# Performance work log

Measured on AMD Instinct MI355X. Metric: run time of the kernel, lower is better.

## Reference

```python
import jax, jax.numpy as jnp
import numpy as np

PRUNE_N = 2  # entries zeroed per group
PRUNE_M = 4  # group size along feature dim


def _prune_2of4(x_flat):
    # x_flat: [N, D]; zero out the PRUNE_N smallest-|.| entries in every
    # contiguous group of PRUNE_M columns (matches torch topk(largest=False)
    # + scatter mask semantics, deterministic sort-order tie-breaking).
    N, D = x_flat.shape
    g = x_flat.reshape(N, D // PRUNE_M, PRUNE_M)           # [N, G, 4]
    a = jnp.abs(g)
    order = jnp.argsort(a, axis=-1)                         # ascending |.|
    rank = jnp.argsort(order, axis=-1)                      # rank of each slot
    keep = rank >= PRUNE_N                                  # keep 2 largest
    return jnp.where(keep, g, jnp.zeros_like(g)).reshape(N, D)


def setup_inputs() -> dict:
    key = jax.random.key(0)
    k1, k2 = jax.random.split(key)
    B, S, D_IN, D_OUT = 2, 4096, 4096, 4096
    x = jax.random.normal(k1, (B, S, D_IN), dtype=jnp.float32)
    weight = jax.random.normal(k2, (D_OUT, D_IN), dtype=jnp.float32) * 0.02
    return {"x": x, "weight": weight}


def reference(x, weight):
    B, S, D = x.shape
    x_flat = x.reshape(B * S, D)
    x_sp = _prune_2of4(x_flat)                              # [B*S, D]
    out = x_sp @ weight.T                                   # [B*S, D_out]
    return out
```

## Files before the change

### kernel.cpp

```cpp
#include <hip/hip_runtime.h>
#include <hip/hip_bf16.h>

typedef float f32x4 __attribute__((ext_vector_type(4)));
typedef __bf16 bf16x8 __attribute__((ext_vector_type(8)));
typedef unsigned short ushort_t;
typedef ushort_t u16x8 __attribute__((ext_vector_type(8)));

__device__ inline ushort_t f2bf_rne(float f) {
  unsigned u = __builtin_bit_cast(unsigned, f);
  unsigned r = (u + 0x7fffu + ((u >> 16) & 1u)) >> 16;
  return (ushort_t)r;
}

__global__ void prune_cast_kernel(const float* __restrict__ x,
                                  ushort_t* __restrict__ xsp, long n8) {
  long i = (long)blockIdx.x * blockDim.x + threadIdx.x;
  if (i >= n8) return;
  const float4* p = reinterpret_cast<const float4*>(x);
  float4 g0 = p[2 * i];
  float4 g1 = p[2 * i + 1];
  float v[8] = {g0.x, g0.y, g0.z, g0.w, g1.x, g1.y, g1.z, g1.w};
  u16x8 o;
#pragma unroll
  for (int g = 0; g < 2; ++g) {
    float a[4];
#pragma unroll
    for (int j = 0; j < 4; ++j) a[j] = fabsf(v[g * 4 + j]);
#pragma unroll
    for (int j = 0; j < 4; ++j) {
      int rank = 0;
#pragma unroll
      for (int k = 0; k < 4; ++k) {
        if (k == j) continue;
        rank += (a[k] < a[j]) || (a[k] == a[j] && k < j);
      }
      o[g * 4 + j] = (rank >= 2) ? f2bf_rne(v[g * 4 + j]) : (ushort_t)0;
    }
  }
  reinterpret_cast<u16x8*>(xsp)[i] = o;
}

__global__ void cast_bf16_kernel(const float* __restrict__ w,
                                 ushort_t* __restrict__ wb, long n8) {
  long i = (long)blockIdx.x * blockDim.x + threadIdx.x;
  if (i >= n8) return;
  const float4* p = reinterpret_cast<const float4*>(w);
  float4 g0 = p[2 * i];
  float4 g1 = p[2 * i + 1];
  u16x8 o;
  o[0] = f2bf_rne(g0.x); o[1] = f2bf_rne(g0.y);
  o[2] = f2bf_rne(g0.z); o[3] = f2bf_rne(g0.w);
  o[4] = f2bf_rne(g1.x); o[5] = f2bf_rne(g1.y);
  o[6] = f2bf_rne(g1.z); o[7] = f2bf_rne(g1.w);
  reinterpret_cast<u16x8*>(wb)[i] = o;
}

#define BARM()                              \
  asm volatile("" ::: "memory");            \
  __builtin_amdgcn_s_barrier();             \
  asm volatile("" ::: "memory");
#define WAIT_VM0() asm volatile("s_waitcnt vmcnt(0)" ::: "memory")

#define STAGE_A(t1, h, par)                                                    \
  {                                                                            \
    const ushort_t* g0 =                                                       \
        A + (a_row0 + (h) * 128 + srow) * (long)Kd + (t1) * 64 + scol;         \
    const ushort_t* g1 =                                                       \
        A + (a_row0 + (h) * 128 + srow + 8) * (long)Kd + (t1) * 64 + scol;     \
    ushort_t* l0 = &ldsA[((par) * 2 + (h)) * 8192 + w * 1024];                 \
    __builtin_amdgcn_global_load_lds(                                          \
        (const __attribute__((address_space(1))) void*)g0,                     \
        (__attribute__((address_space(3))) void*)l0, 16, 0, 0);                \
    __builtin_amdgcn_global_load_lds(                                          \
        (const __attribute__((address_space(1))) void*)g1,                     \
        (__attribute__((address_space(3))) void*)(l0 + 512), 16, 0, 0);        \
  }

#define STAGE_B(t1, h, par)                                                    \
  {                                                                            \
    const ushort_t* g0 =                                                       \
        B + (b_row0 + (h) * 128 + srow) * (long)Kd + (t1) * 64 + scol;         \
    const ushort_t* g1 =                                                       \
        B + (b_row0 + (h) * 128 + srow + 8) * (long)Kd + (t1) * 64 + scol;     \
    ushort_t* l0 = &ldsB[((par) * 2 + (h)) * 8192 + w * 1024];                 \
    __builtin_amdgcn_global_load_lds(                                          \
        (const __attribute__((address_space(1))) void*)g0,                     \
        (__attribute__((address_space(3))) void*)l0, 16, 0, 0);                \
    __builtin_amdgcn_global_load_lds(                                          \
        (const __attribute__((address_space(1))) void*)g1,                     \
        (__attribute__((address_space(3))) void*)(l0 + 512), 16, 0, 0);        \
  }

#define LDA_FRAG(dst, par, mi, s)                                              \
  dst = *reinterpret_cast<const bf16x8*>(                                      \
      reinterpret_cast<const char*>(ldsA) + ((par) * 2 + wr) * 16384 +         \
      (mi) * 2048 + ((s) ? roff1 : roff0));

#define LDB_FRAG(dst, par, ni, s)                                              \
  dst = *reinterpret_cast<const bf16x8*>(                                      \
      reinterpret_cast<const char*>(ldsB) + ((par) * 2 + (wc >> 1)) * 16384 +  \
      (wc & 1) * 8192 + (ni) * 2048 + ((s) ? roff1 : roff0));

#define MFMA_Q(MH, NH)                                                         \
  __builtin_amdgcn_s_setprio(1);                                               \
  _Pragma("unroll") for (int s = 0; s < 2; ++s)                                \
  _Pragma("unroll") for (int mi = 0; mi < 4; ++mi)                             \
  _Pragma("unroll") for (int ni = 0; ni < 2; ++ni)                             \
      acc[(MH) * 4 + mi][(NH) * 2 + ni] =                                      \
          __builtin_amdgcn_mfma_f32_16x16x32_bf16(                             \
              af[mi][s], bfr[(NH) * 2 + ni][s],                                \
              acc[(MH) * 4 + mi][(NH) * 2 + ni], 0, 0, 0);                     \
  __builtin_amdgcn_s_setprio(0);

#define KTILE(t, PAR)                                                          \
  {                                                                            \
    const int tN = ((t) + 1 < NT) ? (t) + 1 : NT - 1;                          \
           \
    STAGE_A(tN, 0, (PAR) ^ 1)                                                  \
    STAGE_A(tN, 1, (PAR) ^ 1)                                                  \
    STAGE_B(tN, 0, (PAR) ^ 1)                                                  \
    STAGE_B(tN, 1, (PAR) ^ 1)                                                  \
                          \
    _Pragma("unroll") for (int mi = 0; mi < 4; ++mi)                           \
    _Pragma("unroll") for (int s = 0; s < 2; ++s)                              \
        LDA_FRAG(af[mi][s], PAR, mi, s)                                        \
    _Pragma("unroll") for (int ni = 0; ni < 4; ++ni)                           \
    _Pragma("unroll") for (int s = 0; s < 2; ++s)                              \
        LDB_FRAG(bfr[ni][s], PAR, ni, s)                                       \
    MFMA_Q(0, 0)                                                               \
    MFMA_Q(0, 1)                                                               \
    _Pragma("unroll") for (int mi = 0; mi < 4; ++mi)                           \
    _Pragma("unroll") for (int s = 0; s < 2; ++s)                              \
        LDA_FRAG(af[mi][s], PAR, 4 + mi, s)                                    \
    MFMA_Q(1, 1)                                                               \
    MFMA_Q(1, 0)                                                               \
    WAIT_VM0();                                                                \
    BARM()                                                                     \
  }

__global__ __launch_bounds__(512, 1) void gemm256_kernel(
    const ushort_t* __restrict__ A,
    const ushort_t* __restrict__ B,
    float* __restrict__ C,
    int M, int N, int Kd) {
  __shared__ ushort_t ldsA[4 * 8192];
  __shared__ ushort_t ldsB[4 * 8192];

  const int tid = threadIdx.x;
  const int lane = tid & 63;
  const int w = tid >> 6;
  const int wr = w >> 2;
  const int wc = w & 3;

  const int b = blockIdx.x;
  const int wg = (b & 7) * (gridDim.x >> 3) + (b >> 3);
  const int nbn = N / 256;
  const int bm = wg / nbn, bn = wg % nbn;
  const long a_row0 = (long)bm * 256;
  const long b_row0 = (long)bn * 256;
  const int NT = Kd / 64;

  const int srow = w * 16 + (lane >> 3);
  const int scol = (((lane & 7) ^ ((lane >> 3) & 7)) << 3);

  const int rl = lane & 15;
  const int q = lane >> 4;
  const int roff0 = rl * 128 + (((q) ^ (rl & 7)) << 4);
  const int roff1 = rl * 128 + (((q | 4) ^ (rl & 7)) << 4);

  f32x4 acc[8][4];
#pragma unroll
  for (int i = 0; i < 8; ++i)
#pragma unroll
    for (int j = 0; j < 4; ++j) acc[i][j] = f32x4{0.f, 0.f, 0.f, 0.f};

  bf16x8 af[4][2];
  bf16x8 bfr[4][2];

  STAGE_A(0, 0, 0)
  STAGE_A(0, 1, 0)
  STAGE_B(0, 0, 0)
  STAGE_B(0, 1, 0)
  WAIT_VM0();
  BARM()

  for (int t = 0; t < NT; t += 2) {
    KTILE(t, 0)
    KTILE(t + 1, 1)
  }

  const int orow = (lane >> 4) * 4;
  const int ocol = lane & 15;
#pragma unroll
  for (int mi = 0; mi < 8; ++mi)
#pragma unroll
    for (int ni = 0; ni < 4; ++ni) {
      const long r0 = a_row0 + wr * 128 + mi * 16 + orow;
      const long c0 = b_row0 + wc * 64 + ni * 16 + ocol;
#pragma unroll
      for (int r = 0; r < 4; ++r) C[(r0 + r) * N + c0] = acc[mi][ni][r];
    }
}

extern "C" void kernel_launch(void* const* d_in, const int* in_sizes, int n_in,
                              void* d_out, int out_size, void* d_ws,
                              size_t ws_size, hipStream_t stream) {
  const float* x = (const float*)d_in[0];
  const float* w = (const float*)d_in[1];
  float* out = (float*)d_out;

  const int K = 4096;
  const long M = (long)in_sizes[0] / K;
  const int N = in_sizes[1] / K;

  ushort_t* xsp = (ushort_t*)d_ws;
  ushort_t* wb = xsp + (long)M * K;

  const long n8x = M * K / 8;
  prune_cast_kernel<<<(int)((n8x + 255) / 256), 256, 0, stream>>>(x, xsp, n8x);

  const long n8w = (long)N * K / 8;
  cast_bf16_kernel<<<(int)((n8w + 255) / 256), 256, 0, stream>>>(w, wb, n8w);

  const int nwg = (int)(M / 256) * (N / 256);
  gemm256_kernel<<<nwg, 512, 0, stream>>>(xsp, wb, out, (int)M, N, K);
}
```

Before: 282.1 us.

## Load B fragments directly from global memory instead of staging through LDS

Removes LDS staging for the weight (B) operand. Each wave now loads its own B MFMA fragments straight from global memory into registers, while A stays double-buffered in LDS. This halves LDS use and drops the B LDS writes and reads, at the cost of more global traffic: B rows are re-read by the two row-waves that share them, loads are uncoalesced 16-byte per lane, and their latency is exposed within the same k-tile with no prefetch. The existing vmcnt(0) wait now also covers the B loads.

Result: slower. 427.8 us (+51.6%).

```diff
diff --git a/kernel.cpp b/kernel.cpp
--- a/kernel.cpp
+++ b/kernel.cpp
@@ -76,30 +76,14 @@
         (__attribute__((address_space(3))) void*)(l0 + 512), 16, 0, 0);        \
   }
 
-#define STAGE_B(t1, h, par)                                                    \
-  {                                                                            \
-    const ushort_t* g0 =                                                       \
-        B + (b_row0 + (h) * 128 + srow) * (long)Kd + (t1) * 64 + scol;         \
-    const ushort_t* g1 =                                                       \
-        B + (b_row0 + (h) * 128 + srow + 8) * (long)Kd + (t1) * 64 + scol;     \
-    ushort_t* l0 = &ldsB[((par) * 2 + (h)) * 8192 + w * 1024];                 \
-    __builtin_amdgcn_global_load_lds(                                          \
-        (const __attribute__((address_space(1))) void*)g0,                     \
-        (__attribute__((address_space(3))) void*)l0, 16, 0, 0);                \
-    __builtin_amdgcn_global_load_lds(                                          \
-        (const __attribute__((address_space(1))) void*)g1,                     \
-        (__attribute__((address_space(3))) void*)(l0 + 512), 16, 0, 0);        \
-  }
-
 #define LDA_FRAG(dst, par, mi, s)                                              \
   dst = *reinterpret_cast<const bf16x8*>(                                      \
       reinterpret_cast<const char*>(ldsA) + ((par) * 2 + wr) * 16384 +         \
       (mi) * 2048 + ((s) ? roff1 : roff0));
 
-#define LDB_FRAG(dst, par, ni, s)                                              \
-  dst = *reinterpret_cast<const bf16x8*>(                                      \
-      reinterpret_cast<const char*>(ldsB) + ((par) * 2 + (wc >> 1)) * 16384 +  \
-      (wc & 1) * 8192 + (ni) * 2048 + ((s) ? roff1 : roff0));
+#define LDB_G(dst, ni, s, t)                                                   \
+  dst = *reinterpret_cast<const bf16x8*>(bpB + (long)(ni) * 16 * Kd +          \
+                                         (t) * 64 + (s) * 32);
 
 #define MFMA_Q(MH, NH)                                                         \
   __builtin_amdgcn_s_setprio(1);                                               \
@@ -114,21 +98,22 @@
 
 #define KTILE(t, PAR)                                                          \
   {                                                                            \
-    const int tN = ((t) + 1 < NT) ? (t) + 1 : NT - 1;                          \
-           \
-    STAGE_A(tN, 0, (PAR) ^ 1)                                                  \
-    STAGE_A(tN, 1, (PAR) ^ 1)                                                  \
-    STAGE_B(tN, 0, (PAR) ^ 1)                                                  \
-    STAGE_B(tN, 1, (PAR) ^ 1)                                                  \
-                          \
+    const int tA = ((t) + 1 < NT) ? (t) + 1 : NT - 1;                          \
+        \
+    LDB_G(bfr[0][0], 0, 0, t) LDB_G(bfr[0][1], 0, 1, t)                        \
+    LDB_G(bfr[1][0], 1, 0, t) LDB_G(bfr[1][1], 1, 1, t)                        \
+    LDB_G(bfr[2][0], 2, 0, t) LDB_G(bfr[2][1], 2, 1, t)                        \
+    LDB_G(bfr[3][0], 3, 0, t) LDB_G(bfr[3][1], 3, 1, t)                        \
+                    \
+    STAGE_A(tA, 0, (PAR) ^ 1)                                                  \
+    STAGE_A(tA, 1, (PAR) ^ 1)                                                  \
+                                        \
     _Pragma("unroll") for (int mi = 0; mi < 4; ++mi)                           \
     _Pragma("unroll") for (int s = 0; s < 2; ++s)                              \
         LDA_FRAG(af[mi][s], PAR, mi, s)                                        \
-    _Pragma("unroll") for (int ni = 0; ni < 4; ++ni)                           \
-    _Pragma("unroll") for (int s = 0; s < 2; ++s)                              \
-        LDB_FRAG(bfr[ni][s], PAR, ni, s)                                       \
     MFMA_Q(0, 0)                                                               \
     MFMA_Q(0, 1)                                                               \
+                                         \
     _Pragma("unroll") for (int mi = 0; mi < 4; ++mi)                           \
     _Pragma("unroll") for (int s = 0; s < 2; ++s)                              \
         LDA_FRAG(af[mi][s], PAR, 4 + mi, s)                                    \
@@ -144,7 +129,6 @@
     float* __restrict__ C,
     int M, int N, int Kd) {
   __shared__ ushort_t ldsA[4 * 8192];
-  __shared__ ushort_t ldsB[4 * 8192];
 
   const int tid = threadIdx.x;
   const int lane = tid & 63;
@@ -168,6 +152,8 @@
   const int roff0 = rl * 128 + (((q) ^ (rl & 7)) << 4);
   const int roff1 = rl * 128 + (((q | 4) ^ (rl & 7)) << 4);
 
+  const ushort_t* bpB = B + (long)(b_row0 + wc * 64 + rl) * Kd + q * 8;
+
   f32x4 acc[8][4];
 #pragma unroll
   for (int i = 0; i < 8; ++i)
@@ -179,8 +165,6 @@
 
   STAGE_A(0, 0, 0)
   STAGE_A(0, 1, 0)
-  STAGE_B(0, 0, 0)
-  STAGE_B(0, 1, 0)
   WAIT_VM0();
   BARM()
 
```
